# Kernel tuning notes

Measured on AMD Instinct MI355X. Metric: run time of the kernel, lower is better.

## Reference

```python
import jax, jax.numpy as jnp
import numpy as np

B, R, C, A, K = 32, 13, 13, 5, 20
CELL = K + 5                      # 4 coords + objectness + 20 classes
N = R * C * A                     # 845 boxes per image
THRESH = 0.5
NMS_TH = 0.4
BIAS_VALS = [1.3221, 1.73145, 3.19275, 4.00944, 5.05587,
             8.09892, 9.47112, 4.84053, 11.2364, 10.0071]


def setup_inputs() -> dict:
    key = jax.random.key(0)
    x = jax.random.normal(key, (B, R, C, A * CELL), dtype=jnp.float32)
    bias = jnp.array(BIAS_VALS, dtype=jnp.float32)  # anchor priors (w,h interleaved)
    return {"x": x, "bias": bias}


def _nms_keep(iou, scores):
    """Greedy per-class NMS. iou: [B,N,N]; scores: [B,K,N] (already thresholded).
    Returns bool keep mask [B,K,N]. Decisions are non-differentiable, so inputs
    are stop_gradient'ed by the caller."""
    Bn = scores.shape[0]
    valid = scores > THRESH
    order = jnp.argsort(-scores, axis=-1)          # descending score order [B,K,N]
    rank = jnp.argsort(order, axis=-1)             # inverse permutation   [B,K,N]
    barange = jnp.arange(Bn)[:, None]

    def body(i, suppressed):
        idx = order[:, :, i]                                              # [B,K]
        sup_i = jnp.take_along_axis(suppressed, idx[:, :, None], -1)[..., 0]
        val_i = jnp.take_along_axis(valid, idx[:, :, None], -1)[..., 0]
        alive = val_i & ~sup_i                                            # [B,K]
        row = iou[barange, idx]                                           # [B,K,N]
        return suppressed | (alive[..., None] & (row > NMS_TH) & (rank > i))

    suppressed = jax.lax.fori_loop(0, N, body, jnp.zeros((Bn, K, N), bool))
    return valid & ~suppressed


def reference(x, bias):
    Bn, R_, C_, _ = x.shape
    t = x.reshape(Bn, R_, C_, A, CELL)
    gx = jnp.arange(C_, dtype=x.dtype)
    gy = jnp.arange(R_, dtype=x.dtype)
    # box decode (matches source: hNorm=rows used for width, wNorm=cols for height)
    bx = (jax.nn.sigmoid(t[..., 0]) + gx[None, None, :, None]) / C_
    by = (jax.nn.sigmoid(t[..., 1]) + gy[None, :, None, None]) / R_
    bw = jnp.exp(t[..., 2]) * bias[0::2] / R_
    bh = jnp.exp(t[..., 3]) * bias[1::2] / C_
    obj = jax.nn.sigmoid(t[..., 4])
    cls = jax.nn.softmax(t[..., 5:], axis=-1)
    prob = obj[..., None] * cls
    prob = jnp.where(prob > THRESH, prob, 0.0)

    # flatten to box index layout (y*cols + x)*anchors + a, same as source
    flat = lambda a: a.reshape(Bn, N)
    bx, by, bw, bh, obj = map(flat, (bx, by, bw, bh, obj))
    prob = prob.reshape(Bn, N, K)

    # corner-form boxes for IoU (source uses x - w/2, y - h/2, w, h)
    x1 = bx - bw * 0.5
    y1 = by - bh * 0.5
    x2 = x1 + bw
    y2 = y1 + bh
    iw = jnp.maximum(0.0, jnp.minimum(x2[:, :, None], x2[:, None, :]) -
                          jnp.maximum(x1[:, :, None], x1[:, None, :]))
    ih = jnp.maximum(0.0, jnp.minimum(y2[:, :, None], y2[:, None, :]) -
                          jnp.maximum(y1[:, :, None], y1[:, None, :]))
    inter = iw * ih
    area = bw * bh
    union = area[:, :, None] + area[:, None, :] - inter
    iou = inter / jnp.maximum(union, 1e-9)                       # [B,N,N]

    scores = prob.transpose(0, 2, 1)                             # [B,K,N]
    keep = _nms_keep(jax.lax.stop_gradient(iou),
                     jax.lax.stop_gradient(scores))
    out_prob = jnp.where(keep, scores, 0.0).transpose(0, 2, 1)   # [B,N,K]

    out = jnp.concatenate([bx[..., None], by[..., None], bw[..., None],
                           bh[..., None], obj[..., None], out_prob], axis=-1)
    return out  # [B, N, CELL]
```

## Files before the change

kernel.cpp:

```cpp
#include <hip/hip_runtime.h>
#include <math.h>

#define BN 32
#define RR 13
#define CC 13
#define AA 5
#define KK 20
#define CELLSZ 25
#define NN (RR * CC * AA)
#define TOT (NN * CELLSZ)
#define THRESH 0.5f
#define NMS_TH 0.4f
#define NT 1024

__global__ __launch_bounds__(NT) void region_kernel(
        const float* __restrict__ x,
        const float* __restrict__ bias,
        float* __restrict__ out)
{
    __shared__ float sraw[TOT];
    __shared__ int   pcnt;
    __shared__ int   kcnt[KK];
    __shared__ int   ctag[NN], cidx[NN];
    __shared__ float csc[NN], px1[NN], py1[NN], px2[NN], py2[NN], par[NN];

    const int b   = blockIdx.x;
    const int tid = threadIdx.x;
    const float* xb = x   + (size_t)b * TOT;
    float*       ob = out + (size_t)b * TOT;

    if (tid == 0) pcnt = 0;
    if (tid < KK) kcnt[tid] = 0;

    for (int i = tid; i < TOT; i += NT) sraw[i] = xb[i];
    __syncthreads();

    if (tid < NN) {
        const int n  = tid;
        int r   = n / (CC * AA);
        int rem = n - r * (CC * AA);
        int c   = rem / AA;
        int a   = rem - c * AA;
        float* t = sraw + n * CELLSZ;

        float bx  = (1.f / (1.f + expf(-t[0])) + (float)c) / (float)CC;
        float by  = (1.f / (1.f + expf(-t[1])) + (float)r) / (float)RR;
        float bw  = expf(t[2]) * bias[2 * a]     / (float)RR;
        float bh  = expf(t[3]) * bias[2 * a + 1] / (float)CC;
        float obj = 1.f / (1.f + expf(-t[4]));

        float l[KK];
        float m = t[5];
#pragma unroll
        for (int k = 0; k < KK; ++k) { l[k] = t[5 + k]; m = fmaxf(m, l[k]); }
        float s = 0.f;
#pragma unroll
        for (int k = 0; k < KK; ++k) s += expf(l[k] - m);
        int km = 0;
#pragma unroll
        for (int k = 1; k < KK; ++k) if (l[k] > l[km]) km = k;

        float p = obj * (1.0f / s);

        t[0] = bx; t[1] = by; t[2] = bw; t[3] = bh; t[4] = obj;
#pragma unroll
        for (int k = 0; k < KK; ++k) t[5 + k] = 0.f;

        if (p > THRESH) {
            int slot = atomicAdd(&pcnt, 1);
            atomicAdd(&kcnt[km], 1);
            ctag[slot] = km; cidx[slot] = n; csc[slot] = p;
            float x1 = bx - bw * 0.5f, y1 = by - bh * 0.5f;
            px1[slot] = x1; py1[slot] = y1;
            px2[slot] = x1 + bw; py2[slot] = y1 + bh;
            par[slot] = bw * bh;
        }
    }
    __syncthreads();

    const int mtot = pcnt;
    const int wave = tid >> 6;
    const int lane = tid & 63;
    const int T    = (mtot + 63) >> 6;

    for (int k = wave; k < KK; k += (NT / 64)) {
        if (kcnt[k] == 0) continue;
        unsigned alive = 0;
        for (int tt = 0; tt < T; ++tt) {
            int j = lane + (tt << 6);
            if (j < mtot && ctag[j] == k) alive |= (1u << tt);
        }
        while (true) {
            float bs = -1.f; int bnn = 0x7fffffff; int bg = -1;
            for (int tt = 0; tt < T; ++tt) {
                if ((alive >> tt) & 1u) {
                    int j = lane + (tt << 6);
                    float sc = csc[j]; int nn = cidx[j];
                    if (sc > bs || (sc == bs && nn < bnn)) { bs = sc; bnn = nn; bg = j; }
                }
            }
#pragma unroll
            for (int off = 32; off; off >>= 1) {
                float os = __shfl_xor(bs, off);
                int   on = __shfl_xor(bnn, off);
                int   og = __shfl_xor(bg, off);
                if (os > bs || (os == bs && on < bnn)) { bs = os; bnn = on; bg = og; }
            }
            if (bg < 0) break;

            float X1 = px1[bg], Y1 = py1[bg], X2 = px2[bg], Y2 = py2[bg], AR = par[bg];
            if ((bg & 63) == lane) {
                sraw[bnn * CELLSZ + 5 + k] = bs;
                alive &= ~(1u << (bg >> 6));
            }
            for (int tt = 0; tt < T; ++tt) {
                int j = lane + (tt << 6);
                if (((alive >> tt) & 1u) && j != bg) {
                    float iw = fmaxf(0.f, fminf(X2, px2[j]) - fmaxf(X1, px1[j]));
                    float ih = fmaxf(0.f, fminf(Y2, py2[j]) - fmaxf(Y1, py1[j]));
                    float inter = iw * ih;
                    float uni   = AR + par[j] - inter;
                    if (inter / fmaxf(uni, 1e-9f) > NMS_TH) alive &= ~(1u << tt);
                }
            }
        }
    }
    __syncthreads();

    for (int i = tid; i < TOT; i += NT) ob[i] = sraw[i];
}

extern "C" void kernel_launch(void* const* d_in, const int* in_sizes, int n_in,
                              void* d_out, int out_size, void* d_ws, size_t ws_size,
                              hipStream_t stream) {
    const float* x    = (const float*)d_in[0];
    const float* bias = (const float*)d_in[1];
    float* out = (float*)d_out;

    region_kernel<<<BN, NT, 0, stream>>>(x, bias, out);
}
```

Before: 65.32 us.

## Split decode into a grid-wide kernel and run NMS in a separate kernel

Result: no change. 65.73 us (+0.6%).

```diff
diff --git a/kernel.cpp b/kernel.cpp
--- a/kernel.cpp
+++ b/kernel.cpp
@@ -11,80 +11,91 @@
 #define TOT (NN * CELLSZ)
 #define THRESH 0.5f
 #define NMS_TH 0.4f
-#define NT 1024
 
-__global__ __launch_bounds__(NT) void region_kernel(
+
+__device__ __forceinline__ float sigmoidf_(float x) {
+    return 1.0f / (1.0f + expf(-x));
+}
+
+__global__ __launch_bounds__(256) void decode_kernel(
         const float* __restrict__ x,
         const float* __restrict__ bias,
-        float* __restrict__ out)
-{
-    __shared__ float sraw[TOT];
+        float* __restrict__ out,
+        float4* __restrict__ recs) {
+    int idx = blockIdx.x * 256 + threadIdx.x;
+    if (idx >= BN * NN) return;
+    int n   = idx % NN;
+    int r   = n / (CC * AA);
+    int rem = n - r * (CC * AA);
+    int c   = rem / AA;
+    int a   = rem - c * AA;
+
+    const float* t = x + (size_t)idx * CELLSZ;
+
+    float bx  = (sigmoidf_(t[0]) + (float)c) / (float)CC;
+    float by  = (sigmoidf_(t[1]) + (float)r) / (float)RR;
+    float bw  = expf(t[2]) * bias[2 * a]     / (float)RR;
+    float bh  = expf(t[3]) * bias[2 * a + 1] / (float)CC;
+    float obj = sigmoidf_(t[4]);
+
+    float l[KK];
+    float m = t[5];
+#pragma unroll
+    for (int k = 0; k < KK; ++k) { l[k] = t[5 + k]; m = fmaxf(m, l[k]); }
+    float s = 0.f;
+#pragma unroll
+    for (int k = 0; k < KK; ++k) s += expf(l[k] - m);
+    int km = 0;
+#pragma unroll
+    for (int k = 1; k < KK; ++k) if (l[k] > l[km]) km = k;
+
+    float p = obj * (1.0f / s);
+
+    float* o = out + (size_t)idx * CELLSZ;
+    o[0] = bx; o[1] = by; o[2] = bw; o[3] = bh; o[4] = obj;
+#pragma unroll
+    for (int k = 0; k < KK; ++k) o[5 + k] = 0.f;
+
+    float x1 = bx - bw * 0.5f, y1 = by - bh * 0.5f;
+    recs[(size_t)idx * 2]     = make_float4(p, __int_as_float(km), x1, y1);
+    recs[(size_t)idx * 2 + 1] = make_float4(x1 + bw, y1 + bh, bw * bh, 0.f);
+}
+
+__global__ __launch_bounds__(1024) void nms_kernel(
+        const float4* __restrict__ recs,
+        float* __restrict__ out) {
     __shared__ int   pcnt;
-    __shared__ int   kcnt[KK];
     __shared__ int   ctag[NN], cidx[NN];
     __shared__ float csc[NN], px1[NN], py1[NN], px2[NN], py2[NN], par[NN];
 
-    const int b   = blockIdx.x;
-    const int tid = threadIdx.x;
-    const float* xb = x   + (size_t)b * TOT;
-    float*       ob = out + (size_t)b * TOT;
+    const int b    = blockIdx.x;
+    const int tid  = threadIdx.x;
+    const int lane = tid & 63;
+    const int wave = tid >> 6;
 
     if (tid == 0) pcnt = 0;
-    if (tid < KK) kcnt[tid] = 0;
-
-    for (int i = tid; i < TOT; i += NT) sraw[i] = xb[i];
     __syncthreads();
 
     if (tid < NN) {
-        const int n  = tid;
-        int r   = n / (CC * AA);
-        int rem = n - r * (CC * AA);
-        int c   = rem / AA;
-        int a   = rem - c * AA;
-        float* t = sraw + n * CELLSZ;
-
-        float bx  = (1.f / (1.f + expf(-t[0])) + (float)c) / (float)CC;
-        float by  = (1.f / (1.f + expf(-t[1])) + (float)r) / (float)RR;
-        float bw  = expf(t[2]) * bias[2 * a]     / (float)RR;
-        float bh  = expf(t[3]) * bias[2 * a + 1] / (float)CC;
-        float obj = 1.f / (1.f + expf(-t[4]));
-
-        float l[KK];
-        float m = t[5];
-#pragma unroll
-        for (int k = 0; k < KK; ++k) { l[k] = t[5 + k]; m = fmaxf(m, l[k]); }
-        float s = 0.f;
-#pragma unroll
-        for (int k = 0; k < KK; ++k) s += expf(l[k] - m);
-        int km = 0;
-#pragma unroll
-        for (int k = 1; k < KK; ++k) if (l[k] > l[km]) km = k;
-
-        float p = obj * (1.0f / s);
-
-        t[0] = bx; t[1] = by; t[2] = bw; t[3] = bh; t[4] = obj;
-#pragma unroll
-        for (int k = 0; k < KK; ++k) t[5 + k] = 0.f;
-
-        if (p > THRESH) {
+        float4 r0 = recs[((size_t)b * NN + tid) * 2];
+        if (r0.x > THRESH) {
+            float4 r1 = recs[((size_t)b * NN + tid) * 2 + 1];
             int slot = atomicAdd(&pcnt, 1);
-            atomicAdd(&kcnt[km], 1);
-            ctag[slot] = km; cidx[slot] = n; csc[slot] = p;
-            float x1 = bx - bw * 0.5f, y1 = by - bh * 0.5f;
-            px1[slot] = x1; py1[slot] = y1;
-            px2[slot] = x1 + bw; py2[slot] = y1 + bh;
-            par[slot] = bw * bh;
+            ctag[slot] = __float_as_int(r0.y);
+            cidx[slot] = tid;
+            csc[slot]  = r0.x;
+            px1[slot]  = r0.z;  py1[slot] = r0.w;
+            px2[slot]  = r1.x;  py2[slot] = r1.y;
+            par[slot]  = r1.z;
         }
     }
     __syncthreads();
 
     const int mtot = pcnt;
-    const int wave = tid >> 6;
-    const int lane = tid & 63;
-    const int T    = (mtot + 63) >> 6;
+    if (mtot == 0) return;
+    const int T = (mtot + 63) >> 6;
 
-    for (int k = wave; k < KK; k += (NT / 64)) {
-        if (kcnt[k] == 0) continue;
+    for (int k = wave; k < KK; k += 16) {
         unsigned alive = 0;
         for (int tt = 0; tt < T; ++tt) {
             int j = lane + (tt << 6);
@@ -110,7 +121,7 @@
 
             float X1 = px1[bg], Y1 = py1[bg], X2 = px2[bg], Y2 = py2[bg], AR = par[bg];
             if ((bg & 63) == lane) {
-                sraw[bnn * CELLSZ + 5 + k] = bs;
+                out[((size_t)b * NN + bnn) * CELLSZ + 5 + k] = bs;
                 alive &= ~(1u << (bg >> 6));
             }
             for (int tt = 0; tt < T; ++tt) {
@@ -125,9 +136,6 @@
             }
         }
     }
-    __syncthreads();
-
-    for (int i = tid; i < TOT; i += NT) ob[i] = sraw[i];
 }
 
 extern "C" void kernel_launch(void* const* d_in, const int* in_sizes, int n_in,
@@ -135,7 +143,9 @@
                               hipStream_t stream) {
     const float* x    = (const float*)d_in[0];
     const float* bias = (const float*)d_in[1];
-    float* out = (float*)d_out;
+    float*  out  = (float*)d_out;
+    float4* recs = (float4*)d_ws;
 
-    region_kernel<<<BN, NT, 0, stream>>>(x, bias, out);
+    decode_kernel<<<(BN * NN + 255) / 256, 256, 0, stream>>>(x, bias, out, recs);
+    nms_kernel<<<BN, 1024, 0, stream>>>(recs, out);
 }
```
